# Optimization experiments

Measured on AMD Instinct MI355X. Metric: run time of the kernel, lower is better.

## Reference

```python
import jax, jax.numpy as jnp
import numpy as np

I = 512
D = 256
C = 10          # num_clusters
E = 8           # cluster_emb_dim
NCLS = 2
NEG = -1e9

def _xavier(key, shape):
    fan_in, fan_out = shape[0], shape[1]
    std = np.sqrt(2.0 / (fan_in + fan_out))
    return jax.random.normal(key, shape, dtype=jnp.float32) * std

def setup_inputs() -> dict:
    key = jax.random.key(0)
    ks = jax.random.split(key, 16)
    B, N = 8, 8192
    h = jax.random.normal(ks[0], (B, N, I), dtype=jnp.float32)
    cluster_ids = jax.random.randint(ks[1], (B, N), 0, C)
    return {
        "h": h,
        "cluster_ids": cluster_ids,
        "emb_table": jax.random.normal(ks[2], (C, E), dtype=jnp.float32) * 0.02,
        "Wf": _xavier(ks[3], (I + E, I)), "bf": jnp.zeros((I,), jnp.float32),
        # intra gated attention
        "Wa": _xavier(ks[4], (I, D)), "ba": jnp.zeros((D,), jnp.float32),
        "Wb": _xavier(ks[5], (I, D)), "bb": jnp.zeros((D,), jnp.float32),
        "Wc": _xavier(ks[6], (D, 1)), "bc": jnp.zeros((1,), jnp.float32),
        "Wfc": _xavier(ks[7], (I, 512)), "bfc": jnp.zeros((512,), jnp.float32),
        # inter gated attention
        "Wa2": _xavier(ks[8], (512, D)), "ba2": jnp.zeros((D,), jnp.float32),
        "Wb2": _xavier(ks[9], (512, D)), "bb2": jnp.zeros((D,), jnp.float32),
        "Wc2": _xavier(ks[10], (D, 1)), "bc2": jnp.zeros((1,), jnp.float32),
        "Wfc2": _xavier(ks[11], (512, 256)), "bfc2": jnp.zeros((256,), jnp.float32),
        "Wcls": _xavier(ks[12], (256, NCLS)), "bcls": jnp.zeros((NCLS,), jnp.float32),
    }

def reference(h, cluster_ids, emb_table, Wf, bf, Wa, ba, Wb, bb, Wc, bc,
              Wfc, bfc, Wa2, ba2, Wb2, bb2, Wc2, bc2, Wfc2, bfc2, Wcls, bcls):
    # 1) fuse cluster embedding: concat + Linear + ReLU  -> [B,N,I]
    emb = emb_table[cluster_ids]                              # [B,N,E]
    x = jnp.concatenate([h, emb], axis=-1)                    # [B,N,I+E]
    x = jax.nn.relu(jnp.einsum('bnf,fi->bni', x, Wf) + bf)    # [B,N,I]

    # 2) intra-cluster gated attention scores (shared MLP over all patches)
    a = jnp.tanh(jnp.einsum('bni,id->bnd', x, Wa) + ba)
    g = jax.nn.sigmoid(jnp.einsum('bni,id->bnd', x, Wb) + bb)
    s = (jnp.einsum('bnd,do->bno', a * g, Wc) + bc)[..., 0]   # [B,N]

    # segmented softmax per (batch, cluster): mask then softmax over N
    m = cluster_ids[:, :, None] == jnp.arange(C)[None, None, :]  # [B,N,C] bool
    sm = jnp.where(m, s[:, :, None], NEG)
    A = jax.nn.softmax(sm, axis=1)                             # [B,N,C]

    # weighted sum per cluster -> [B,C,I], then intra_fc -> [B,C,512]
    cfeat = jnp.einsum('bnc,bni->bci', A, x)
    cfeat = jax.nn.relu(jnp.einsum('bci,io->bco', cfeat, Wfc) + bfc)

    # 3) inter-cluster gated attention over C clusters
    a2 = jnp.tanh(jnp.einsum('bcf,fd->bcd', cfeat, Wa2) + ba2)
    g2 = jax.nn.sigmoid(jnp.einsum('bcf,fd->bcd', cfeat, Wb2) + bb2)
    s2 = (jnp.einsum('bcd,do->bco', a2 * g2, Wc2) + bc2)[..., 0]  # [B,C]
    A2 = jax.nn.softmax(s2, axis=1)                               # [B,C]
    slide = jnp.einsum('bc,bcf->bf', A2, cfeat)                   # [B,512]
    slide = jax.nn.relu(slide @ Wfc2 + bfc2)                      # [B,256]

    # 4) classifier
    logits = slide @ Wcls + bcls                                  # [B,n_classes]
    return logits
```

## Files before the change

### kernel.cpp

```cpp
#include <hip/hip_runtime.h>
#include <math.h>

#define B_    8
#define N_    8192
#define M_    65536
#define I_    512
#define E_    8
#define D_    256
#define C_    10
#define NCLS_ 2

typedef unsigned short ushort_t;
typedef ushort_t ushortx8 __attribute__((ext_vector_type(8)));
typedef __bf16   bf16x8  __attribute__((ext_vector_type(8)));
typedef float    f32x4   __attribute__((ext_vector_type(4)));

static const size_t XB_OFF   = 0;
static const size_t PS_OFF   = 67108864;
static const size_t S_OFF    = PS_OFF + 2097152;
static const size_t STAT_OFF = S_OFF + 262144;
static const size_t PST_OFF  = STAT_OFF + 1024;
static const size_t CP_OFF   = PST_OFF + 5120;
static const size_t CF_OFF   = CP_OFF + 10485760;
static const size_t CF2_OFF  = CF_OFF + 163840;
static const size_t S2_OFF   = CF2_OFF + 163840;
static const size_t WFT_OFF  = S2_OFF + 512;
static const size_t BAG_OFF  = WFT_OFF + 524288;
static const size_t EMBW_OFF = BAG_OFF + 524288;

__device__ __forceinline__ float sigf(float v) { return 1.0f / (1.0f + __expf(-v)); }

__device__ __forceinline__ ushort_t f2bf(float f) {
    union { float f; unsigned u; } v; v.f = f;
    unsigned r = v.u + 0x7FFF + ((v.u >> 16) & 1);
    return (ushort_t)(r >> 16);
}
__device__ __forceinline__ float bf2f(ushort_t u) {
    union { unsigned u; float f; } v; v.u = ((unsigned)u) << 16; return v.f;
}

__device__ __forceinline__ void gl_lds16(const void* g, void* l) {
    __builtin_amdgcn_global_load_lds(
        (const __attribute__((address_space(1))) void*)g,
        (__attribute__((address_space(3))) void*)l, 16, 0, 0);
}

__global__ __launch_bounds__(256) void prep_kernel(
    const float* __restrict__ Wf, const float* __restrict__ Wa,
    const float* __restrict__ Wb, const float* __restrict__ emb,
    const float* __restrict__ bfv,
    ushort_t* __restrict__ wft, ushort_t* __restrict__ bag,
    float* __restrict__ embW)
{
    const int bid = blockIdx.x;
    const int t = threadIdx.x;
    if (bid < 1024) {
        int idx = bid * 256 + t;
        int k = idx >> 9, n = idx & 511;
        wft[(size_t)n * 512 + k] = f2bf(Wf[(size_t)k * 512 + n]);
    } else if (bid < 1536) {
        int idx = (bid - 1024) * 256 + t;
        int k = idx >> 8, d = idx & 255;
        float a = Wa[(size_t)k * 256 + d];
        float g = Wb[(size_t)k * 256 + d];
        int blk = d >> 5, w = d & 31;
        bag[(size_t)(blk * 64 + w) * 512 + k]      = f2bf(a);
        bag[(size_t)(blk * 64 + 32 + w) * 512 + k] = f2bf(g);
    } else {
        int idx = (bid - 1536) * 256 + t;
        int c = idx >> 9, n = idx & 511;
        float s = bfv[n];
#pragma unroll
        for (int e = 0; e < 8; ++e) s += emb[c * 8 + e] * Wf[(size_t)(512 + e) * 512 + n];
        embW[(size_t)c * 512 + n] = s;
    }
}

__global__ __launch_bounds__(512) void gemm_x_mfma(
    const float* __restrict__ hf, const int* __restrict__ cid,
    const ushort_t* __restrict__ wft, const float* __restrict__ embW,
    ushort_t* __restrict__ xb)
{
    __shared__ float    Asf[2][256 * 32];
    __shared__ ushort_t Bs[2][128 * 32];

    const int t = threadIdx.x;
    const int lin = blockIdx.y * 4 + blockIdx.x;
    const int swz = (lin & 7) * 128 + (lin >> 3);
    const int n0 = (swz & 3) * 128;
    const int m0 = (swz >> 2) * 256;

    const int wid = t >> 6;
    const int wr = wid >> 1, wc = wid & 1;
    const int l = t & 63, lr = l & 15, lg = l >> 4;

    const int srow = l >> 2;
    const int gchB = ((l & 3) ^ ((l >> 3) & 3)) * 8;
    const size_t gB0 = (size_t)(n0 + wid * 16 + srow) * 512 + gchB;
    ushort_t* lB = &Bs[0][wid * 512];

    const int ArowL = wid * 32 + (l >> 3);
    const int gchA  = ((l & 7) ^ ((l >> 3) & 7)) * 4;
    const size_t gAf = (size_t)(m0 + ArowL) * 512 + gchA;

    f32x4 acc[4][4] = {};

#define STAGE_X(buf, kt) do { \
    size_t ko = (size_t)(kt) * 32; \
    char* aB = (char*)&Asf[buf][0] + wid * 4096; \
    gl_lds16(hf + gAf + ko,            aB); \
    gl_lds16(hf + gAf + ko +  8 * 512, aB + 1024); \
    gl_lds16(hf + gAf + ko + 16 * 512, aB + 2048); \
    gl_lds16(hf + gAf + ko + 24 * 512, aB + 3072); \
    gl_lds16(wft + gB0 + ko, lB + (buf) * 4096); \
} while (0)

    STAGE_X(0, 0);
    __syncthreads();
    int cur = 0;
    for (int kt = 0; kt < 16; ++kt) {
        if (kt < 15) STAGE_X(cur ^ 1, kt + 1);
        const float* Aw = &Asf[cur][0];
        const char*  Bb = (const char*)&Bs[cur][0];
        bf16x8 af[4], bg[4];
#pragma unroll
        for (int mi = 0; mi < 4; ++mi) {
            int R = wr * 64 + mi * 16 + lr;
            const float* Arow = Aw + R * 32;
            int s7 = R & 7;
            f32x4 lo = *(const f32x4*)(Arow + (((2 * lg)     ^ s7) << 2));
            f32x4 hi = *(const f32x4*)(Arow + (((2 * lg + 1) ^ s7) << 2));
            bf16x8 a;
            a[0] = (__bf16)lo[0]; a[1] = (__bf16)lo[1];
            a[2] = (__bf16)lo[2]; a[3] = (__bf16)lo[3];
            a[4] = (__bf16)hi[0]; a[5] = (__bf16)hi[1];
            a[6] = (__bf16)hi[2]; a[7] = (__bf16)hi[3];
            af[mi] = a;
        }
#pragma unroll
        for (int ni = 0; ni < 4; ++ni) {
            int Cc = wc * 64 + ni * 16 + lr;
            bg[ni] = *(const bf16x8*)(Bb + Cc * 64 + ((lg ^ ((Cc >> 1) & 3)) << 4));
        }
#pragma unroll
        for (int mi = 0; mi < 4; ++mi)
#pragma unroll
            for (int ni = 0; ni < 4; ++ni)
                acc[mi][ni] = __builtin_amdgcn_mfma_f32_16x16x32_bf16(af[mi], bg[ni], acc[mi][ni], 0, 0, 0);
        __syncthreads();
        cur ^= 1;
    }

#pragma unroll
    for (int mi = 0; mi < 4; ++mi) {
#pragma unroll
        for (int r = 0; r < 4; ++r) {
            int row = m0 + wr * 64 + mi * 16 + lg * 4 + r;
            const float* ew = embW + (size_t)cid[row] * 512;
#pragma unroll
            for (int ni = 0; ni < 4; ++ni) {
                int col = n0 + wc * 64 + ni * 16 + lr;
                float v = acc[mi][ni][r] + ew[col];
                xb[(size_t)row * 512 + col] = f2bf(fmaxf(v, 0.0f));
            }
        }
    }
}

__global__ __launch_bounds__(512) void gemm_ag_mfma(
    const ushort_t* __restrict__ xb, const ushort_t* __restrict__ bag,
    const float* __restrict__ bav, const float* __restrict__ bbv,
    const float* __restrict__ Wc, float* __restrict__ ps)
{
    __shared__ ushort_t As[2][256 * 32];
    __shared__ ushort_t Bs[2][128 * 32];

    const int t = threadIdx.x;
    const int lin = blockIdx.y * 4 + blockIdx.x;
    const int swz = (lin & 7) * 128 + (lin >> 3);
    const int bxn = swz & 3;
    const int n0 = bxn * 128;
    const int m0 = (swz >> 2) * 256;

    const int wid = t >> 6;
    const int wr = wid >> 1, wc = wid & 1;
    const int l = t & 63, lr = l & 15, lg = l >> 4;

    const int srow = l >> 2;
    const int gch  = ((l & 3) ^ ((l >> 3) & 3)) * 8;

    const size_t gA0 = (size_t)(m0 + wid * 32 + srow) * 512 + gch;
    const size_t gA1 = gA0 + 16 * 512;
    const size_t gB0 = (size_t)(n0 + wid * 16 + srow) * 512 + gch;
    ushort_t* lA = &As[0][wid * 1024];
    ushort_t* lB = &Bs[0][wid * 512];

    f32x4 acc[4][4] = {};

#define STAGE_AG(buf, kt) do { \
    size_t ko = (size_t)(kt) * 32; \
    gl_lds16(xb + gA0 + ko,  lA + (buf) * 8192); \
    gl_lds16(xb + gA1 + ko,  lA + (buf) * 8192 + 512); \
    gl_lds16(bag + gB0 + ko, lB + (buf) * 4096); \
} while (0)

    STAGE_AG(0, 0);
    __syncthreads();
    int cur = 0;
    for (int kt = 0; kt < 16; ++kt) {
        if (kt < 15) STAGE_AG(cur ^ 1, kt + 1);
        const char* Ab = (const char*)&As[cur][0];
        const char* Bb = (const char*)&Bs[cur][0];
        bf16x8 af[4], bg[4];
#pragma unroll
        for (int mi = 0; mi < 4; ++mi) {
            int R = wr * 64 + mi * 16 + lr;
            af[mi] = *(const bf16x8*)(Ab + R * 64 + ((lg ^ ((R >> 1) & 3)) << 4));
        }
#pragma unroll
        for (int ni = 0; ni < 4; ++ni) {
            int Cc = wc * 64 + ni * 16 + lr;
            bg[ni] = *(const bf16x8*)(Bb + Cc * 64 + ((lg ^ ((Cc >> 1) & 3)) << 4));
        }
#pragma unroll
        for (int mi = 0; mi < 4; ++mi)
#pragma unroll
            for (int ni = 0; ni < 4; ++ni)
                acc[mi][ni] = __builtin_amdgcn_mfma_f32_16x16x32_bf16(af[mi], bg[ni], acc[mi][ni], 0, 0, 0);
        __syncthreads();
        cur ^= 1;
    }

    const int blk = bxn * 2 + wc;
    const int d0 = blk * 32 + lr, d1 = d0 + 16;
    const float ba0 = bav[d0], ba1 = bav[d1];
    const float bb0 = bbv[d0], bb1 = bbv[d1];
    const float w0 = Wc[d0],  w1 = Wc[d1];

#pragma unroll
    for (int mi = 0; mi < 4; ++mi) {
#pragma unroll
        for (int r = 0; r < 4; ++r) {
            float p = tanhf(acc[mi][0][r] + ba0) * sigf(acc[mi][2][r] + bb0) * w0
                    + tanhf(acc[mi][1][r] + ba1) * sigf(acc[mi][3][r] + bb1) * w1;
            p += __shfl_xor(p, 1); p += __shfl_xor(p, 2);
            p += __shfl_xor(p, 4); p += __shfl_xor(p, 8);
            if (lr == 0)
                ps[(size_t)blk * M_ + m0 + wr * 64 + mi * 16 + lg * 4 + r] = p;
        }
    }
}

__global__ __launch_bounds__(256) void sstats_kernel(
    const float* __restrict__ ps, const float* __restrict__ bc,
    const int* __restrict__ cid, float* __restrict__ S,
    float* __restrict__ pst)
{
    __shared__ float redm[4][C_];
    __shared__ float smx[C_];
    __shared__ float reds[4][C_];

    const int b  = blockIdx.x >> 3;
    const int sl = blockIdx.x & 7;
    const int bs = blockIdx.x;
    const int t  = threadIdx.x;
    const int l  = t & 63, wv = t >> 6;
    const int base = b * N_ + sl * 1024;

    float sv[4]; int cv[4];
#pragma unroll
    for (int i = 0; i < 4; ++i) {
        int m = base + i * 256 + t;
        float v = bc[0];
#pragma unroll
        for (int k = 0; k < 8; ++k) v += ps[(size_t)k * M_ + m];
        S[m] = v; sv[i] = v; cv[i] = cid[m];
    }

    float mx[C_];
#pragma unroll
    for (int c = 0; c < C_; ++c) mx[c] = -3.0e38f;
#pragma unroll
    for (int i = 0; i < 4; ++i)
#pragma unroll
        for (int c = 0; c < C_; ++c)
            mx[c] = fmaxf(mx[c], (cv[i] == c) ? sv[i] : -3.0e38f);
#pragma unroll
    for (int c = 0; c < C_; ++c) {
        float v = mx[c];
        v = fmaxf(v, __shfl_xor(v, 32)); v = fmaxf(v, __shfl_xor(v, 16));
        v = fmaxf(v, __shfl_xor(v, 8));  v = fmaxf(v, __shfl_xor(v, 4));
        v = fmaxf(v, __shfl_xor(v, 2));  v = fmaxf(v, __shfl_xor(v, 1));
        if (l == 0) redm[wv][c] = v;
    }
    __syncthreads();
    if (t < C_)
        smx[t] = fmaxf(fmaxf(redm[0][t], redm[1][t]), fmaxf(redm[2][t], redm[3][t]));
    __syncthreads();

    float sm[C_];
#pragma unroll
    for (int c = 0; c < C_; ++c) sm[c] = 0.f;
#pragma unroll
    for (int i = 0; i < 4; ++i) {
        float e = expf(sv[i] - smx[cv[i]]);
#pragma unroll
        for (int c = 0; c < C_; ++c) sm[c] += (cv[i] == c) ? e : 0.f;
    }
#pragma unroll
    for (int c = 0; c < C_; ++c) {
        float v = sm[c];
        v += __shfl_xor(v, 32); v += __shfl_xor(v, 16); v += __shfl_xor(v, 8);
        v += __shfl_xor(v, 4);  v += __shfl_xor(v, 2);  v += __shfl_xor(v, 1);
        if (l == 0) reds[wv][c] = v;
    }
    __syncthreads();
    if (t < C_) {
        pst[bs * C_ + t]       = smx[t];
        pst[640 + bs * C_ + t] = reds[0][t] + reds[1][t] + reds[2][t] + reds[3][t];
    }
}

__global__ void stats2_kernel(const float* __restrict__ pst, float* __restrict__ stat)
{
    int t = threadIdx.x;
    if (t < 80) {
        int b = t / C_, c = t % C_;
        float mxv = -3.0e38f;
#pragma unroll
        for (int sl = 0; sl < 8; ++sl)
            mxv = fmaxf(mxv, pst[(b * 8 + sl) * C_ + c]);
        float sum = 0.f;
#pragma unroll
        for (int sl = 0; sl < 8; ++sl)
            sum += pst[640 + (b * 8 + sl) * C_ + c] * expf(pst[(b * 8 + sl) * C_ + c] - mxv);
        stat[t]      = mxv;
        stat[80 + t] = 1.0f / sum;
    }
}

__global__ __launch_bounds__(256) void cpart_kernel(
    const ushort_t* __restrict__ xb, const int* __restrict__ cid,
    const float* __restrict__ s, const float* __restrict__ stat,
    float* __restrict__ cpart)
{
    __shared__ float wrow[128];
    __shared__ int   crow[128];
    const int b     = blockIdx.x >> 6;
    const int chunk = blockIdx.x & 63;
    const int t     = threadIdx.x;
    const int base  = b * N_ + chunk * 128;

    if (t < 128) {
        int m = base + t;
        int c = cid[m];
        crow[t] = c;
        wrow[t] = expf(s[m] - stat[b * C_ + c]) * stat[80 + b * C_ + c];
    }
    __syncthreads();

    float2 acc[C_];
#pragma unroll
    for (int c = 0; c < C_; ++c) { acc[c].x = 0.f; acc[c].y = 0.f; }

    for (int r = 0; r < 128; ++r) {
        int c = crow[r];
        float wv = wrow[r];
        unsigned xv = *(const unsigned*)(xb + (size_t)(base + r) * 512 + t * 2);
        float x0 = bf2f((ushort_t)(xv & 0xffff));
        float x1 = bf2f((ushort_t)(xv >> 16));
#pragma unroll
        for (int cc = 0; cc < C_; ++cc) {
            float w = (cc == c) ? wv : 0.0f;
            acc[cc].x += w * x0;
            acc[cc].y += w * x1;
        }
    }
#pragma unroll
    for (int cc = 0; cc < C_; ++cc)
        *(float2*)(&cpart[(((size_t)blockIdx.x) * C_ + cc) * 512 + t * 2]) = acc[cc];
}

__global__ void creduce_kernel(const float* __restrict__ cpart, float* __restrict__ cfeat)
{
    int o = blockIdx.x * 256 + threadIdx.x;
    int i = o & 511;
    int bc = o >> 9;
    int b = bc / C_, c = bc % C_;
    float sum = 0.f;
    for (int ch = 0; ch < 64; ++ch)
        sum += cpart[(((size_t)(b * 64 + ch)) * C_ + c) * 512 + i];
    cfeat[o] = sum;
}

__global__ __launch_bounds__(256) void intra_inter_kernel(
    const float* __restrict__ cfeat, const float* __restrict__ Wfc,
    const float* __restrict__ bfc,
    const float* __restrict__ Wa2, const float* __restrict__ ba2,
    const float* __restrict__ Wb2, const float* __restrict__ bb2,
    const float* __restrict__ Wc2, const float* __restrict__ bc2,
    float* __restrict__ cfeat2, float* __restrict__ s2)
{
    __shared__ float row[512];
    __shared__ float row2[512];
    __shared__ float red[256];
    const int bc = blockIdx.x;
    const int t  = threadIdx.x;
    row[t] = cfeat[bc * 512 + t]; row[t + 256] = cfeat[bc * 512 + 256 + t];
    __syncthreads();
    float a0 = 0.f, a1 = 0.f;
    for (int i = 0; i < 512; ++i) {
        float rv = row[i];
        a0 += rv * Wfc[(size_t)i * 512 + t];
        a1 += rv * Wfc[(size_t)i * 512 + 256 + t];
    }
    a0 = fmaxf(a0 + bfc[t], 0.f);
    a1 = fmaxf(a1 + bfc[256 + t], 0.f);
    cfeat2[bc * 512 + t]       = a0;
    cfeat2[bc * 512 + 256 + t] = a1;
    row2[t] = a0; row2[t + 256] = a1;
    __syncthreads();

    float pa = 0.f, pg = 0.f;
    for (int f = 0; f < 512; ++f) {
        float rv = row2[f];
        pa += rv * Wa2[(size_t)f * 256 + t];
        pg += rv * Wb2[(size_t)f * 256 + t];
    }
    float v = tanhf(pa + ba2[t]) * sigf(pg + bb2[t]) * Wc2[t];
    red[t] = v; __syncthreads();
    for (int off = 128; off > 0; off >>= 1) {
        if (t < off) red[t] += red[t + off];
        __syncthreads();
    }
    if (t == 0) s2[bc] = red[0] + bc2[0];
}

__global__ __launch_bounds__(256) void final_kernel(
    const float* __restrict__ cfeat2, const float* __restrict__ s2,
    const float* __restrict__ Wfc2, const float* __restrict__ bfc2,
    const float* __restrict__ Wcls, const float* __restrict__ bcls,
    float* __restrict__ out)
{
    __shared__ float A2[C_];
    __shared__ float slide[512];
    __shared__ float slide2[256];
    const int b = blockIdx.x;
    const int t = threadIdx.x;

    if (t < C_) A2[t] = s2[b * C_ + t];
    __syncthreads();
    float mx = -3.0e38f;
    for (int c = 0; c < C_; ++c) mx = fmaxf(mx, A2[c]);
    float sum = 0.f;
    for (int c = 0; c < C_; ++c) sum += expf(A2[c] - mx);
    __syncthreads();
    if (t < C_) A2[t] = expf(A2[t] - mx) / sum;
    __syncthreads();

    float s0 = 0.f, s1 = 0.f;
    for (int c = 0; c < C_; ++c) {
        float a = A2[c];
        s0 += a * cfeat2[(b * C_ + c) * 512 + t];
        s1 += a * cfeat2[(b * C_ + c) * 512 + 256 + t];
    }
    slide[t] = s0; slide[t + 256] = s1;
    __syncthreads();

    float acc = 0.f;
    for (int f = 0; f < 512; ++f) acc += slide[f] * Wfc2[(size_t)f * 256 + t];
    slide2[t] = fmaxf(acc + bfc2[t], 0.f);
    __syncthreads();

    if (t < NCLS_) {
        float lg = bcls[t];
        for (int o = 0; o < 256; ++o) lg += slide2[o] * Wcls[o * 2 + t];
        out[b * 2 + t] = lg;
    }
}

extern "C" void kernel_launch(void* const* d_in, const int* in_sizes, int n_in,
                              void* d_out, int out_size, void* d_ws, size_t ws_size,
                              hipStream_t stream)
{
    (void)in_sizes; (void)n_in; (void)out_size; (void)ws_size;
    const float* h    = (const float*)d_in[0];
    const int*   cid  = (const int*)  d_in[1];
    const float* emb  = (const float*)d_in[2];
    const float* Wf   = (const float*)d_in[3];
    const float* bf   = (const float*)d_in[4];
    const float* Wa   = (const float*)d_in[5];
    const float* ba   = (const float*)d_in[6];
    const float* Wb   = (const float*)d_in[7];
    const float* bb   = (const float*)d_in[8];
    const float* Wc   = (const float*)d_in[9];
    const float* bc   = (const float*)d_in[10];
    const float* Wfc  = (const float*)d_in[11];
    const float* bfc  = (const float*)d_in[12];
    const float* Wa2  = (const float*)d_in[13];
    const float* ba2  = (const float*)d_in[14];
    const float* Wb2  = (const float*)d_in[15];
    const float* bb2  = (const float*)d_in[16];
    const float* Wc2  = (const float*)d_in[17];
    const float* bc2  = (const float*)d_in[18];
    const float* Wfc2 = (const float*)d_in[19];
    const float* bfc2 = (const float*)d_in[20];
    const float* Wcls = (const float*)d_in[21];
    const float* bcls = (const float*)d_in[22];

    char* ws = (char*)d_ws;
    ushort_t* XB   = (ushort_t*)(ws + XB_OFF);
    float* PS      = (float*)(ws + PS_OFF);
    float* S       = (float*)(ws + S_OFF);
    float* STAT    = (float*)(ws + STAT_OFF);
    float* PST     = (float*)(ws + PST_OFF);
    float* CPART   = (float*)(ws + CP_OFF);
    float* CFEAT   = (float*)(ws + CF_OFF);
    float* CFEAT2  = (float*)(ws + CF2_OFF);
    float* S2      = (float*)(ws + S2_OFF);
    ushort_t* WFT  = (ushort_t*)(ws + WFT_OFF);
    ushort_t* BAG  = (ushort_t*)(ws + BAG_OFF);
    float* EMBW    = (float*)(ws + EMBW_OFF);
    float* out     = (float*)d_out;

    prep_kernel<<<1556, 256, 0, stream>>>(Wf, Wa, Wb, emb, bf, WFT, BAG, EMBW);

    gemm_x_mfma<<<dim3(4, 256), 512, 0, stream>>>(h, cid, WFT, EMBW, XB);
    gemm_ag_mfma<<<dim3(4, 256), 512, 0, stream>>>(XB, BAG, ba, bb, Wc, PS);

    sstats_kernel<<<64, 256, 0, stream>>>(PS, bc, cid, S, PST);
    stats2_kernel<<<1, 128, 0, stream>>>(PST, STAT);
    cpart_kernel<<<512, 256, 0, stream>>>(XB, cid, S, STAT, CPART);
    creduce_kernel<<<160, 256, 0, stream>>>(CPART, CFEAT);
    intra_inter_kernel<<<B_ * C_, 256, 0, stream>>>(CFEAT, Wfc, bfc,
                                                    Wa2, ba2, Wb2, bb2, Wc2, bc2,
                                                    CFEAT2, S2);
    final_kernel<<<B_, 256, 0, stream>>>(CFEAT2, S2, Wfc2, bfc2, Wcls, bcls, out);
}
```

Baseline: 223.4 us.

## Prefetch two K-tiles ahead with explicit vmcnt waits in both GEMM loops

Both double-buffered GEMM mainloops now issue two stages of global-to-LDS loads up front. Each iteration waits with a partial s_waitcnt vmcnt instead of a full __syncthreads drain, so one stage's loads stay in flight during compute. After the MFMAs, an LDS wait and a barrier guard the buffer before the next-next tile is issued into it. The intent is to hide more global load latency, at the cost of hand-tuned counter values that depend on how many loads each stage issues.

```diff
diff --git a/kernel.cpp b/kernel.cpp
--- a/kernel.cpp
+++ b/kernel.cpp
@@ -44,6 +44,12 @@
         (const __attribute__((address_space(1))) void*)g,
         (__attribute__((address_space(3))) void*)l, 16, 0, 0);
 }
+
+#define VMWAIT5 asm volatile("s_waitcnt vmcnt(5)" ::: "memory")
+#define VMWAIT3 asm volatile("s_waitcnt vmcnt(3)" ::: "memory")
+#define VMWAIT0 asm volatile("s_waitcnt vmcnt(0)" ::: "memory")
+#define LGWAIT0 asm volatile("s_waitcnt lgkmcnt(0)" ::: "memory")
+#define SFENCE  asm volatile("" ::: "memory")
 
 __global__ __launch_bounds__(256) void prep_kernel(
     const float* __restrict__ Wf, const float* __restrict__ Wa,
@@ -116,12 +122,12 @@
 } while (0)
 
     STAGE_X(0, 0);
-    __syncthreads();
-    int cur = 0;
+    STAGE_X(1, 1);
     for (int kt = 0; kt < 16; ++kt) {
-        if (kt < 15) STAGE_X(cur ^ 1, kt + 1);
-        const float* Aw = &Asf[cur][0];
-        const char*  Bb = (const char*)&Bs[cur][0];
+        if (kt < 15) { VMWAIT5; } else { VMWAIT0; }
+        __builtin_amdgcn_s_barrier(); SFENCE;
+        const float* Aw = &Asf[kt & 1][0];
+        const char*  Bb = (const char*)&Bs[kt & 1][0];
         bf16x8 af[4], bg[4];
 #pragma unroll
         for (int mi = 0; mi < 4; ++mi) {
@@ -147,8 +153,9 @@
 #pragma unroll
             for (int ni = 0; ni < 4; ++ni)
                 acc[mi][ni] = __builtin_amdgcn_mfma_f32_16x16x32_bf16(af[mi], bg[ni], acc[mi][ni], 0, 0, 0);
-        __syncthreads();
-        cur ^= 1;
+        LGWAIT0;
+        __builtin_amdgcn_s_barrier(); SFENCE;
+        if (kt + 2 < 16) STAGE_X(kt & 1, kt + 2);
     }
 
 #pragma unroll
@@ -205,12 +212,12 @@
 } while (0)
 
     STAGE_AG(0, 0);
-    __syncthreads();
-    int cur = 0;
+    STAGE_AG(1, 1);
     for (int kt = 0; kt < 16; ++kt) {
-        if (kt < 15) STAGE_AG(cur ^ 1, kt + 1);
-        const char* Ab = (const char*)&As[cur][0];
-        const char* Bb = (const char*)&Bs[cur][0];
+        if (kt < 15) { VMWAIT3; } else { VMWAIT0; }
+        __builtin_amdgcn_s_barrier(); SFENCE;
+        const char* Ab = (const char*)&As[kt & 1][0];
+        const char* Bb = (const char*)&Bs[kt & 1][0];
         bf16x8 af[4], bg[4];
 #pragma unroll
         for (int mi = 0; mi < 4; ++mi) {
@@ -227,8 +234,9 @@
 #pragma unroll
             for (int ni = 0; ni < 4; ++ni)
                 acc[mi][ni] = __builtin_amdgcn_mfma_f32_16x16x32_bf16(af[mi], bg[ni], acc[mi][ni], 0, 0, 0);
-        __syncthreads();
-        cur ^= 1;
+        LGWAIT0;
+        __builtin_amdgcn_s_barrier(); SFENCE;
+        if (kt + 2 < 16) STAGE_AG(kt & 1, kt + 2);
     }
 
     const int blk = bxn * 2 + wc;
```

Measured after the change: 247.0 us. 10.5% more time.

## Stage GEMM epilogue through LDS and fold stats/reduce kernels into neighbors

Applied to the files above, without the earlier changes.

The first GEMM's epilogue now writes bf16 results into shared memory, then stores them to global as 16-byte vectors instead of scattered 2-byte stores. The stats2 kernel is removed: each cpart block recomputes the per-cluster max and inverse sum from the partial stats. The creduce kernel is folded into intra_inter, which sums the 64 chunk partials itself. Together these cut two launches and an intermediate buffer, at the cost of redundant stat computation and a slower serial reduction inside 80 blocks.

```diff
diff --git a/kernel.cpp b/kernel.cpp
--- a/kernel.cpp
+++ b/kernel.cpp
@@ -18,11 +18,9 @@
 static const size_t XB_OFF   = 0;
 static const size_t PS_OFF   = 67108864;
 static const size_t S_OFF    = PS_OFF + 2097152;
-static const size_t STAT_OFF = S_OFF + 262144;
-static const size_t PST_OFF  = STAT_OFF + 1024;
+static const size_t PST_OFF  = S_OFF + 262144;
 static const size_t CP_OFF   = PST_OFF + 5120;
-static const size_t CF_OFF   = CP_OFF + 10485760;
-static const size_t CF2_OFF  = CF_OFF + 163840;
+static const size_t CF2_OFF  = CP_OFF + 10485760;
 static const size_t S2_OFF   = CF2_OFF + 163840;
 static const size_t WFT_OFF  = S2_OFF + 512;
 static const size_t BAG_OFF  = WFT_OFF + 524288;
@@ -151,18 +149,30 @@
         cur ^= 1;
     }
 
+    ushort_t* sc = (ushort_t*)&Asf[0][0];
 #pragma unroll
     for (int mi = 0; mi < 4; ++mi) {
 #pragma unroll
         for (int r = 0; r < 4; ++r) {
-            int row = m0 + wr * 64 + mi * 16 + lg * 4 + r;
-            const float* ew = embW + (size_t)cid[row] * 512;
+            int row = wr * 64 + mi * 16 + lg * 4 + r;
+            const float* ew = embW + (size_t)cid[m0 + row] * 512;
 #pragma unroll
             for (int ni = 0; ni < 4; ++ni) {
-                int col = n0 + wc * 64 + ni * 16 + lr;
-                float v = acc[mi][ni][r] + ew[col];
-                xb[(size_t)row * 512 + col] = f2bf(fmaxf(v, 0.0f));
+                int col = wc * 64 + ni * 16 + lr;
+                float v = acc[mi][ni][r] + ew[n0 + col];
+                sc[row * 128 + col] = f2bf(fmaxf(v, 0.0f));
             }
+        }
+    }
+    __syncthreads();
+    {
+        const int cch = t & 15;
+        const int r0  = t >> 4;
+#pragma unroll
+        for (int j = 0; j < 8; ++j) {
+            int row = r0 + j * 32;
+            *(ushortx8*)(xb + (size_t)(m0 + row) * 512 + n0 + cch * 8) =
+                *(const ushortx8*)(sc + row * 128 + cch * 8);
         }
     }
 }
@@ -321,29 +331,12 @@
     }
 }
 
-__global__ void stats2_kernel(const float* __restrict__ pst, float* __restrict__ stat)
-{
-    int t = threadIdx.x;
-    if (t < 80) {
-        int b = t / C_, c = t % C_;
-        float mxv = -3.0e38f;
-#pragma unroll
-        for (int sl = 0; sl < 8; ++sl)
-            mxv = fmaxf(mxv, pst[(b * 8 + sl) * C_ + c]);
-        float sum = 0.f;
-#pragma unroll
-        for (int sl = 0; sl < 8; ++sl)
-            sum += pst[640 + (b * 8 + sl) * C_ + c] * expf(pst[(b * 8 + sl) * C_ + c] - mxv);
-        stat[t]      = mxv;
-        stat[80 + t] = 1.0f / sum;
-    }
-}
-
 __global__ __launch_bounds__(256) void cpart_kernel(
     const ushort_t* __restrict__ xb, const int* __restrict__ cid,
-    const float* __restrict__ s, const float* __restrict__ stat,
+    const float* __restrict__ s, const float* __restrict__ pst,
     float* __restrict__ cpart)
 {
+    __shared__ float smax[C_], sinv[C_];
     __shared__ float wrow[128];
     __shared__ int   crow[128];
     const int b     = blockIdx.x >> 6;
@@ -351,11 +344,24 @@
     const int t     = threadIdx.x;
     const int base  = b * N_ + chunk * 128;
 
+    if (t < C_) {
+        float mxv = -3.0e38f;
+#pragma unroll
+        for (int sl = 0; sl < 8; ++sl)
+            mxv = fmaxf(mxv, pst[(b * 8 + sl) * C_ + t]);
+        float sum = 0.f;
+#pragma unroll
+        for (int sl = 0; sl < 8; ++sl)
+            sum += pst[640 + (b * 8 + sl) * C_ + t] * expf(pst[(b * 8 + sl) * C_ + t] - mxv);
+        smax[t] = mxv;
+        sinv[t] = 1.0f / sum;
+    }
+    __syncthreads();
     if (t < 128) {
         int m = base + t;
         int c = cid[m];
         crow[t] = c;
-        wrow[t] = expf(s[m] - stat[b * C_ + c]) * stat[80 + b * C_ + c];
+        wrow[t] = expf(s[m] - smax[c]) * sinv[c];
     }
     __syncthreads();
 
@@ -381,20 +387,8 @@
         *(float2*)(&cpart[(((size_t)blockIdx.x) * C_ + cc) * 512 + t * 2]) = acc[cc];
 }
 
-__global__ void creduce_kernel(const float* __restrict__ cpart, float* __restrict__ cfeat)
-{
-    int o = blockIdx.x * 256 + threadIdx.x;
-    int i = o & 511;
-    int bc = o >> 9;
-    int b = bc / C_, c = bc % C_;
-    float sum = 0.f;
-    for (int ch = 0; ch < 64; ++ch)
-        sum += cpart[(((size_t)(b * 64 + ch)) * C_ + c) * 512 + i];
-    cfeat[o] = sum;
-}
-
 __global__ __launch_bounds__(256) void intra_inter_kernel(
-    const float* __restrict__ cfeat, const float* __restrict__ Wfc,
+    const float* __restrict__ cpart, const float* __restrict__ Wfc,
     const float* __restrict__ bfc,
     const float* __restrict__ Wa2, const float* __restrict__ ba2,
     const float* __restrict__ Wb2, const float* __restrict__ bb2,
@@ -405,9 +399,18 @@
     __shared__ float row2[512];
     __shared__ float red[256];
     const int bc = blockIdx.x;
+    const int b = bc / C_, c = bc % C_;
     const int t  = threadIdx.x;
-    row[t] = cfeat[bc * 512 + t]; row[t + 256] = cfeat[bc * 512 + 256 + t];
-    __syncthreads();
+
+    float r0 = 0.f, r1 = 0.f;
+    for (int ch = 0; ch < 64; ++ch) {
+        size_t o = (((size_t)(b * 64 + ch)) * C_ + c) * 512;
+        r0 += cpart[o + t];
+        r1 += cpart[o + 256 + t];
+    }
+    row[t] = r0; row[t + 256] = r1;
+    __syncthreads();
+
     float a0 = 0.f, a1 = 0.f;
     for (int i = 0; i < 512; ++i) {
         float rv = row[i];
@@ -512,10 +515,8 @@
     ushort_t* XB   = (ushort_t*)(ws + XB_OFF);
     float* PS      = (float*)(ws + PS_OFF);
     float* S       = (float*)(ws + S_OFF);
-    float* STAT    = (float*)(ws + STAT_OFF);
     float* PST     = (float*)(ws + PST_OFF);
     float* CPART   = (float*)(ws + CP_OFF);
-    float* CFEAT   = (float*)(ws + CF_OFF);
     float* CFEAT2  = (float*)(ws + CF2_OFF);
     float* S2      = (float*)(ws + S2_OFF);
     ushort_t* WFT  = (ushort_t*)(ws + WFT_OFF);
@@ -529,10 +530,8 @@
     gemm_ag_mfma<<<dim3(4, 256), 512, 0, stream>>>(XB, BAG, ba, bb, Wc, PS);
 
     sstats_kernel<<<64, 256, 0, stream>>>(PS, bc, cid, S, PST);
-    stats2_kernel<<<1, 128, 0, stream>>>(PST, STAT);
-    cpart_kernel<<<512, 256, 0, stream>>>(XB, cid, S, STAT, CPART);
-    creduce_kernel<<<160, 256, 0, stream>>>(CPART, CFEAT);
-    intra_inter_kernel<<<B_ * C_, 256, 0, stream>>>(CFEAT, Wfc, bfc,
+    cpart_kernel<<<512, 256, 0, stream>>>(XB, cid, S, PST, CPART);
+    intra_inter_kernel<<<B_ * C_, 256, 0, stream>>>(CPART, Wfc, bfc,
                                                     Wa2, ba2, Wb2, bb2, Wc2, bc2,
                                                     CFEAT2, S2);
     final_kernel<<<B_, 256, 0, stream>>>(CFEAT2, S2, Wfc2, bfc2, Wcls, bcls, out);
```

Result: no change. 226.8 us (+1.5%).
